# Performance work log

Hardware: AMD Instinct MI355X
Metric: run time of the kernel (lower is better)

Reference implementation:

```python
import jax, jax.numpy as jnp
import numpy as np

PRE_NMS_TOPK = 6000
POST_NMS_TOPK = 1000
NMS_THRESH = 0.7
MIN_SIZE = 16.0
NEG = -1e9  # stand-in for -inf that is safe under autodiff


def setup_inputs() -> dict:
    key = jax.random.key(0)
    k1, k2, k3, k4, k5, k6, k7, k8 = jax.random.split(key, 8)
    B, A = 8, 200000
    N = B * A
    # realistic anchors: centers within a ~1333x800 canvas, sizes 16..256
    cx = jax.random.uniform(k1, (N,), minval=0.0, maxval=1200.0)
    cy = jax.random.uniform(k2, (N,), minval=0.0, maxval=800.0)
    w = jax.random.uniform(k3, (N,), minval=16.0, maxval=256.0)
    h = jax.random.uniform(k4, (N,), minval=16.0, maxval=256.0)
    anchors = jnp.stack([cx - 0.5 * w, cy - 0.5 * h, cx + 0.5 * w, cy + 0.5 * h], axis=1)
    batch_indices = jnp.sort(jax.random.randint(k5, (N,), 0, B)).astype(jnp.int32)
    image_sizes = jax.random.randint(k6, (B, 2), 600, 1334).astype(jnp.int32)  # (H, W)
    objectness_logits = jax.random.normal(k7, (N, 1), dtype=jnp.float32)
    bbox_deltas = jax.random.normal(k8, (N, 4), dtype=jnp.float32) * 0.2
    return {
        'anchors': anchors,
        'batch_indices': batch_indices,
        'image_sizes': image_sizes,
        'objectness_logits': objectness_logits,
        'bbox_deltas': bbox_deltas,
    }


def _nms_one(bx, sc):
    """Greedy NMS on [K,4] boxes / [K] scores; returns POST_NMS_TOPK (idx, ok)."""
    K = bx.shape[0]
    areas = (bx[:, 2] - bx[:, 0]) * (bx[:, 3] - bx[:, 1])
    ar = jnp.arange(K)

    def step(sup, _):
        s = jnp.where(sup, NEG, sc)
        j = jnp.argmax(s)
        ok = s[j] > 0.5 * NEG
        b = bx[j]
        ix1 = jnp.maximum(b[0], bx[:, 0])
        iy1 = jnp.maximum(b[1], bx[:, 1])
        ix2 = jnp.minimum(b[2], bx[:, 2])
        iy2 = jnp.minimum(b[3], bx[:, 3])
        inter = jnp.maximum(ix2 - ix1, 0.0) * jnp.maximum(iy2 - iy1, 0.0)
        iou = inter / (areas + areas[j] - inter + 1e-9)
        sup = sup | (iou > NMS_THRESH) | (ar == j)
        return sup, (j, ok)

    sup0 = sc <= 0.5 * NEG  # padded / invalid entries start suppressed
    _, (idx, ok) = jax.lax.scan(step, sup0, None, length=POST_NMS_TOPK)
    return idx, ok


def reference(anchors, batch_indices, image_sizes, objectness_logits, bbox_deltas):
    B = image_sizes.shape[0]
    N = anchors.shape[0]
    sizes = image_sizes[batch_indices].astype(jnp.float32)  # [N,2] (H,W) per anchor

    # --- box decode ---
    a_w = anchors[:, 2] - anchors[:, 0]
    a_h = anchors[:, 3] - anchors[:, 1]
    a_x = anchors[:, 0] + 0.5 * a_w
    a_y = anchors[:, 1] + 0.5 * a_h
    t_x, t_y = bbox_deltas[:, 0], bbox_deltas[:, 1]
    t_w, t_h = bbox_deltas[:, 2], bbox_deltas[:, 3]
    p_x = a_x + t_x * a_w
    p_y = a_y + t_y * a_h
    p_w = a_w * jnp.exp(jnp.clip(t_w, -10.0, 10.0))
    p_h = a_h * jnp.exp(jnp.clip(t_h, -10.0, 10.0))
    x1 = p_x - 0.5 * p_w
    y1 = p_y - 0.5 * p_h
    x2 = p_x + 0.5 * p_w
    y2 = p_y + 0.5 * p_h

    # --- clip to image ---
    H, W = sizes[:, 0], sizes[:, 1]
    x1 = jnp.clip(x1, 0.0, W - 1.0)
    y1 = jnp.clip(y1, 0.0, H - 1.0)
    x2 = jnp.clip(x2, 0.0, W - 1.0)
    y2 = jnp.clip(y2, 0.0, H - 1.0)
    boxes = jnp.stack([x1, y1, x2, y2], axis=1)  # [N,4]

    # --- min-size filter (as score masking) ---
    valid = ((x2 - x1) >= MIN_SIZE) & ((y2 - y1) >= MIN_SIZE)
    fg = jax.nn.sigmoid(objectness_logits[:, 0])

    # --- per-image top-k over masked scores ---
    img_mask = batch_indices[None, :] == jnp.arange(B, dtype=batch_indices.dtype)[:, None]  # [B,N]
    scores = jnp.where(img_mask & valid[None, :], fg[None, :], NEG)  # [B,N]
    top_scores, top_idx = jax.lax.top_k(scores, PRE_NMS_TOPK)  # [B,PRE]
    top_boxes = boxes[top_idx]  # [B,PRE,4]

    # --- NMS per image ---
    keep_idx, keep_ok = jax.vmap(_nms_one)(top_boxes, top_scores)  # [B,POST]

    sel = jnp.take_along_axis(top_idx, keep_idx, axis=1)  # global anchor indices [B,POST]
    okf = keep_ok[..., None].astype(boxes.dtype)
    props = jnp.take_along_axis(top_boxes, keep_idx[..., None], axis=1) * okf  # [B,POST,4]
    obj = objectness_logits[sel] * okf  # [B,POST,1]
    deltas_out = bbox_deltas[sel] * okf  # [B,POST,4]
    bidx = jnp.where(keep_ok, jnp.arange(B, dtype=jnp.int32)[:, None], -1)  # [B,POST]

    return (props.reshape(-1, 4), bidx.reshape(-1), obj.reshape(-1, 1),
            deltas_out.reshape(-1, 4), keep_ok.reshape(-1))
```

## Files before the change

### kernel.cpp

```cpp
#include <hip/hip_runtime.h>
#include <stdint.h>

#define PRE_K   6000
#define POST_K  1000
#define CAP     8192
#define BINS    1024
#define ROWS    6016
#define CH      94
#define RC_CH   32
#define JSPLIT  4
#define NEGF    -1000000000.0f
#define IOU_EPS 16.0f


__device__ __forceinline__ uint32_t orderf(float f) {
  uint32_t u = __float_as_uint(f);
  return (u & 0x80000000u) ? ~u : (u | 0x80000000u);
}

__device__ __forceinline__ int score_bin(float sc) {
  int bin = (int)floorf((sc + 12.0f) * ((float)BINS / 24.0f));
  return bin < 0 ? 0 : (bin > BINS - 1 ? BINS - 1 : bin);
}

__device__ __forceinline__ int bin_slot(int bin) {
  return ((bin & 15) << 6) | (bin >> 4);
}

__device__ __forceinline__ void decode_box(
    const float* __restrict__ anchors, const float* __restrict__ deltas,
    const int* __restrict__ isz, int n, int b,
    double& x1, double& y1, double& x2, double& y2, bool& valid) {
  double ax1 = (double)anchors[4 * n + 0], ay1 = (double)anchors[4 * n + 1];
  double ax2 = (double)anchors[4 * n + 2], ay2 = (double)anchors[4 * n + 3];
  double aw = ax2 - ax1, ah = ay2 - ay1;
  double acx = ax1 + 0.5 * aw, acy = ay1 + 0.5 * ah;
  double tx = (double)deltas[4 * n + 0], ty = (double)deltas[4 * n + 1];
  double tw = (double)deltas[4 * n + 2], th = (double)deltas[4 * n + 3];
  tw = tw < -10.0 ? -10.0 : (tw > 10.0 ? 10.0 : tw);
  th = th < -10.0 ? -10.0 : (th > 10.0 ? 10.0 : th);
  double px = acx + tx * aw, py = acy + ty * ah;
  double pw = aw * exp(tw), ph = ah * exp(th);
  double H = (double)isz[2 * b + 0], W = (double)isz[2 * b + 1];
  double wm = W - 1.0, hm = H - 1.0;
  x1 = px - 0.5 * pw; y1 = py - 0.5 * ph;
  x2 = px + 0.5 * pw; y2 = py + 0.5 * ph;
  x1 = fmin(fmax(x1, 0.0), wm); x2 = fmin(fmax(x2, 0.0), wm);
  y1 = fmin(fmax(y1, 0.0), hm); y2 = fmin(fmax(y2, 0.0), hm);
  valid = (x2 - x1 >= 16.0) && (y2 - y1 >= 16.0);
}

__device__ __forceinline__ bool iou_exact(const double* __restrict__ tbox,
                                          const double* __restrict__ tarea,
                                          size_t ri, size_t ci) {
  const double* pr = &tbox[ri * 4];
  const double* pc = &tbox[ci * 4];
  double w = fmin(pr[2], pc[2]) - fmax(pr[0], pc[0]); w = w > 0.0 ? w : 0.0;
  double h = fmin(pr[3], pc[3]) - fmax(pr[1], pc[1]); h = h > 0.0 ? h : 0.0;
  double it = w * h;
  return it > 0.7 * (tarea[ri] + tarea[ci] - it + 1e-9);
}


__global__ void k_init(uint32_t* hist, uint32_t* cnt, uint32_t* prank, int B) {
  int i = blockIdx.x * blockDim.x + threadIdx.x;
  if (i < B * BINS) hist[i] = 0u;
  if (i < B) cnt[i] = 0u;
  if (i < B * CAP) prank[i] = 0u;
}

__global__ void __launch_bounds__(256) k_score(const float* __restrict__ anchors,
                                               const int* __restrict__ bix,
                                               const int* __restrict__ isz,
                                               const float* __restrict__ logits,
                                               const float* __restrict__ deltas,
                                               float* __restrict__ scores,
                                               uint32_t* __restrict__ hist, int N) {
  const int SPAN = 4096;
  int start = blockIdx.x * SPAN;
  int end = start + SPAN < N ? start + SPAN : N;
  __shared__ uint32_t lh[2][BINS];
  for (int i = threadIdx.x; i < 2 * BINS; i += 256) ((uint32_t*)lh)[i] = 0u;
  __shared__ int s_b0, s_b1;
  if (threadIdx.x == 0) { s_b0 = bix[start]; s_b1 = bix[end - 1]; }
  __syncthreads();
  int b0 = s_b0, b1 = s_b1;

  for (int n = start + (int)threadIdx.x; n < end; n += 256) {
    int b = bix[n];
    double x1, y1, x2, y2; bool valid;
    decode_box(anchors, deltas, isz, n, b, x1, y1, x2, y2, valid);
    float sc = valid ? logits[n] : NEGF;
    scores[n] = sc;
    if (valid) {
      int bin = score_bin(sc);
      if (b == b0)      atomicAdd(&lh[0][bin], 1u);
      else if (b == b1) atomicAdd(&lh[1][bin], 1u);
      else              atomicAdd(&hist[b * BINS + bin_slot(bin)], 1u);
    }
  }
  __syncthreads();
  for (int bin = threadIdx.x; bin < BINS; bin += 256) {
    uint32_t c0 = lh[0][bin];
    if (c0) atomicAdd(&hist[b0 * BINS + bin_slot(bin)], c0);
    if (b1 != b0) {
      uint32_t c1 = lh[1][bin];
      if (c1) atomicAdd(&hist[b1 * BINS + bin_slot(bin)], c1);
    }
  }
}

__global__ void k_scan(const uint32_t* __restrict__ hist, uint32_t* __restrict__ bstar) {
  __shared__ uint32_t s[BINS];
  __shared__ int bs;
  int b = blockIdx.x, t = threadIdx.x;
  s[t] = hist[b * BINS + bin_slot(t)];
  if (t == 0) bs = 0;
  __syncthreads();
  for (int off = 1; off < BINS; off <<= 1) {
    uint32_t v = (t + off < BINS) ? s[t + off] : 0u;
    __syncthreads();
    s[t] += v;
    __syncthreads();
  }
  if (s[t] >= PRE_K) atomicMax(&bs, t);
  __syncthreads();
  if (t == 0) bstar[b] = (uint32_t)bs;
}

__global__ void __launch_bounds__(1024) k_compact(const float* __restrict__ scores,
                                                  const int* __restrict__ bix,
                                                  const uint32_t* __restrict__ bstar,
                                                  uint32_t* __restrict__ cnt,
                                                  uint64_t* __restrict__ cand, int N) {
  const int SPAN = 8192;
  int start = blockIdx.x * SPAN;
  int end = start + SPAN < N ? start + SPAN : N;
  __shared__ uint32_t lcnt[8], lbase[8];
  if (threadIdx.x < 8) lcnt[threadIdx.x] = 0u;
  __syncthreads();

  bool     predv[8];
  uint64_t keyv[8];
  uint32_t lposv[8];
  int      bv[8];
  int nt = 0;
  for (int base = start; base < end; base += 1024, nt++) {
    int n = base + (int)threadIdx.x;
    bool pred = false; int b = 0; uint64_t key = 0ull; uint32_t lp = 0u;
    if (n < end) {
      float sc = scores[n];
      if (sc > 0.5f * NEGF) {
        b = bix[n];
        if ((uint32_t)score_bin(sc) >= bstar[b]) {
          pred = true;
          key = ((uint64_t)orderf(sc) << 32) | (uint64_t)(uint32_t)(~(uint32_t)n);
          lp = atomicAdd(&lcnt[b], 1u);
        }
      }
    }
    predv[nt] = pred; keyv[nt] = key; lposv[nt] = lp; bv[nt] = b;
  }
  __syncthreads();
  if (threadIdx.x < 8) {
    uint32_t c = lcnt[threadIdx.x];
    lbase[threadIdx.x] = c ? atomicAdd(&cnt[threadIdx.x], c) : 0u;
  }
  __syncthreads();
  for (int k = 0; k < nt; k++) {
    if (predv[k]) {
      uint32_t pos = lbase[bv[k]] + lposv[k];
      if (pos < CAP) cand[(size_t)bv[k] * CAP + pos] = keyv[k];
    }
  }
}

__global__ void __launch_bounds__(256) k_rank(const uint64_t* __restrict__ cand,
                                              const uint32_t* __restrict__ cnt,
                                              uint32_t* __restrict__ prank) {
  int blk = blockIdx.x;
  int js = blk % JSPLIT;
  int ic = (blk / JSPLIT) % 32;
  int b  = blk / (JSPLIT * 32);
  int t = threadIdx.x;
  int C = (int)min(cnt[b], (uint32_t)CAP);
  if (ic * 256 >= C) return;
  const uint64_t* g = cand + (size_t)b * CAP;
  int i = ic * 256 + t;
  uint64_t ki = (i < C) ? g[i] : 0ull;

  int q = (C + JSPLIT - 1) / JSPLIT;
  int j0 = js * q;
  int j1 = j0 + q < C ? j0 + q : C;
  if (j0 >= j1) return;

  __shared__ uint64_t tile[1024];
  int rank = 0;
  for (int base = j0; base < j1; base += 1024) {
#pragma unroll
    for (int u = 0; u < 4; u++) {
      int j = base + u * 256 + t;
      tile[u * 256 + t] = (j < j1) ? g[j] : 0ull;
    }
    __syncthreads();
    int lim = j1 - base < 1024 ? j1 - base : 1024;
    const ulonglong2* t2 = (const ulonglong2*)tile;
    int pairs = lim >> 1;
    int jj = 0;
    for (; jj + 4 <= pairs; jj += 4) {
      ulonglong2 v0 = t2[jj + 0], v1 = t2[jj + 1];
      ulonglong2 v2 = t2[jj + 2], v3 = t2[jj + 3];
      rank += (v0.x > ki) ? 1 : 0; rank += (v0.y > ki) ? 1 : 0;
      rank += (v1.x > ki) ? 1 : 0; rank += (v1.y > ki) ? 1 : 0;
      rank += (v2.x > ki) ? 1 : 0; rank += (v2.y > ki) ? 1 : 0;
      rank += (v3.x > ki) ? 1 : 0; rank += (v3.y > ki) ? 1 : 0;
    }
    for (; jj < pairs; jj++) {
      ulonglong2 v = t2[jj];
      rank += (v.x > ki) ? 1 : 0; rank += (v.y > ki) ? 1 : 0;
    }
    if (lim & 1) rank += (tile[lim - 1] > ki) ? 1 : 0;
    __syncthreads();
  }
  if (i < C && rank) atomicAdd(&prank[b * CAP + i], (uint32_t)rank);
}

__global__ void __launch_bounds__(256) k_place(const uint64_t* __restrict__ cand,
                                               const uint32_t* __restrict__ cnt,
                                               const uint32_t* __restrict__ prank,
                                               int* __restrict__ sorted_n,
                                               int* __restrict__ Cnum, int B) {
  int idx = blockIdx.x * blockDim.x + threadIdx.x;
  if (idx >= B * CAP) return;
  int b = idx / CAP, i = idx % CAP;
  int C = (int)min(cnt[b], (uint32_t)CAP);
  if (i == 0) Cnum[b] = C < PRE_K ? C : PRE_K;
  if (i >= C) return;
  uint32_t rank = prank[idx];
  if (rank < PRE_K)
    sorted_n[b * PRE_K + rank] =
        (int)(~(uint32_t)(cand[(size_t)b * CAP + i] & 0xFFFFFFFFull));
}

__global__ void k_gather(const float* __restrict__ anchors,
                         const float* __restrict__ deltas,
                         const int* __restrict__ isz,
                         const int* __restrict__ sorted_n,
                         const int* __restrict__ Cnum,
                         double* __restrict__ tbox, double* __restrict__ tarea,
                         float4* __restrict__ tboxf, float* __restrict__ tareaf,
                         int* __restrict__ top_n, int B) {
  int idx = blockIdx.x * blockDim.x + threadIdx.x;
  if (idx >= B * PRE_K) return;
  int b = idx / PRE_K, r = idx % PRE_K;
  if (r >= Cnum[b]) return;
  int n = sorted_n[idx];
  double x1, y1, x2, y2; bool valid;
  decode_box(anchors, deltas, isz, n, b, x1, y1, x2, y2, valid);
  size_t row = (size_t)b * ROWS + r;
  tbox[row * 4 + 0] = x1;
  tbox[row * 4 + 1] = y1;
  tbox[row * 4 + 2] = x2;
  tbox[row * 4 + 3] = y2;
  double ar = (x2 - x1) * (y2 - y1);
  tarea[row] = ar;
  tboxf[row] = make_float4((float)x1, (float)y1, (float)x2, (float)y2);
  tareaf[row] = (float)ar;
  top_n[idx] = n;
}

__global__ void __launch_bounds__(64) k_iou_mat(const float4* __restrict__ tboxf,
                                                const float* __restrict__ tareaf,
                                                const double* __restrict__ tbox,
                                                const double* __restrict__ tarea,
                                                const int* __restrict__ Cnum,
                                                uint32_t* __restrict__ maskT) {
  int blk = blockIdx.x;
  int k  = blk % (RC_CH + 1);
  int cc = (blk / (RC_CH + 1)) % CH;
  int b  = blk / ((RC_CH + 1) * CH);
  int rc = (k == RC_CH) ? cc : k;
  if (k < RC_CH && cc <= rc) return;
  int C = Cnum[b];
  if (rc * 64 >= C || cc * 64 >= C) return;
  int lane = threadIdx.x;
  size_t bb = (size_t)b * ROWS;

  float4 cb4 = tboxf[bb + (size_t)cc * 64 + lane];
  float  cba = tareaf[bb + (size_t)cc * 64 + lane];
  __shared__ float4 rbx[64];
  __shared__ float  rba[64];
  rbx[lane] = tboxf[bb + (size_t)rc * 64 + lane];
  rba[lane] = tareaf[bb + (size_t)rc * 64 + lane];
  __syncthreads();

  uint32_t* seg = maskT + (((size_t)b * CH + cc) * ROWS + (size_t)rc * 64) * 2;
  bool isdiag = (rc == cc);

  for (int i = 0; i < 64; i++) {
    float4 r4 = rbx[i];
    float ra = rba[i];
    float iw = fminf(r4.z, cb4.z) - fmaxf(r4.x, cb4.x);
    float ih = fminf(r4.w, cb4.w) - fmaxf(r4.y, cb4.y);
    iw = fmaxf(iw, 0.0f); ih = fmaxf(ih, 0.0f);
    float inter = iw * ih;
    float diff = inter - 0.7f * (ra + cba - inter);
    bool gt = isdiag ? (lane > i) : true;
    unsigned long long sup   = __ballot(gt && (diff >  IOU_EPS));
    unsigned long long loose = __ballot(gt && (diff > -IOU_EPS));
    unsigned long long border = loose & ~sup;
    if (border) {
      bool mine = (border >> lane) & 1ull;
      bool ex = false;
      if (mine)
        ex = iou_exact(tbox, tarea, bb + (size_t)rc * 64 + i,
                       bb + (size_t)cc * 64 + lane);
      sup |= __ballot(ex);
    }
    if (lane == 0) {
      seg[i * 2 + 0] = (uint32_t)sup;
      seg[i * 2 + 1] = (uint32_t)(sup >> 32);
    }
  }
}

__global__ void __launch_bounds__(256) k_nms_reduce(const uint32_t* __restrict__ maskT,
                                                    const float4* __restrict__ tboxf,
                                                    const float* __restrict__ tareaf,
                                                    const double* __restrict__ tbox,
                                                    const double* __restrict__ tarea,
                                                    const int* __restrict__ Cnum,
                                                    int* __restrict__ keep,
                                                    int* __restrict__ kept_count) {
  int b = blockIdx.x, t = threadIdx.x;
  int wave = t >> 6, lane = t & 63;
  int C = Cnum[b];
  const uint32_t* M = maskT + (size_t)b * CH * ROWS * 2;
  size_t bb = (size_t)b * ROWS;

  __shared__ uint32_t s_f[2][2];
  __shared__ uint32_t kept_lo[POST_K];
  __shared__ uint32_t kept_hi[POST_K];
  __shared__ uint64_t s_kept;
  if (t < 4) ((uint32_t*)s_f)[t] = 0u;

  uint32_t d0 = 0u, d1 = 0u;
  if (wave == 0) {
    const uint32_t* rp = M + (size_t)lane * 2;
    d0 = rp[0]; d1 = rp[1];
  }
  __syncthreads();

  int nkept = 0, nlo = 0, nhi = 0;
  for (int c = 0; c < CH; c++) {
    int base = c * 64;
    if (base >= C) break;
    int cbuf = c & 1;
    if (t == 0) { s_f[cbuf ^ 1][0] = 0u; s_f[cbuf ^ 1][1] = 0u; }

    uint32_t f0 = 0u, f1 = 0u;
    for (int k2 = t; k2 < nlo; k2 += 256) {
      const uint32_t* rp = M + ((size_t)c * ROWS + kept_lo[k2]) * 2;
      f0 |= rp[0]; f1 |= rp[1];
    }
    if (wave == 1 && nhi > 0) {
      float4 cb4 = tboxf[bb + base + lane];
      float  cba = tareaf[bb + base + lane];
      for (int k2 = 0; k2 < nhi; k2++) {
        int r = (int)kept_hi[k2];
        float4 r4 = tboxf[bb + r];
        float ra = tareaf[bb + r];
        float iw = fminf(r4.z, cb4.z) - fmaxf(r4.x, cb4.x);
        float ih = fminf(r4.w, cb4.w) - fmaxf(r4.y, cb4.y);
        iw = fmaxf(iw, 0.0f); ih = fmaxf(ih, 0.0f);
        float inter = iw * ih;
        float diff = inter - 0.7f * (ra + cba - inter);
        unsigned long long sup   = __ballot(diff >  IOU_EPS);
        unsigned long long loose = __ballot(diff > -IOU_EPS);
        unsigned long long border = loose & ~sup;
        if (border) {
          bool mine = (border >> lane) & 1ull;
          bool ex = false;
          if (mine) ex = iou_exact(tbox, tarea, bb + r, bb + base + lane);
          sup |= __ballot(ex);
        }
        f0 |= (uint32_t)sup; f1 |= (uint32_t)(sup >> 32);
      }
    }
#pragma unroll
    for (int off = 32; off > 0; off >>= 1) {
      f0 |= (uint32_t)__shfl_xor((int)f0, off, 64);
      f1 |= (uint32_t)__shfl_xor((int)f1, off, 64);
    }
    if (lane == 0 && (f0 | f1)) {
      atomicOr(&s_f[cbuf][0], f0);
      atomicOr(&s_f[cbuf][1], f1);
    }
    __syncthreads();

    if (wave == 0) {
      uint64_t sup = (uint64_t)s_f[cbuf][0] | ((uint64_t)s_f[cbuf][1] << 32);
      int rem = C - base;
      if (rem < 64) sup |= ~((1ull << rem) - 1ull);
      uint64_t diag = (uint64_t)d0 | ((uint64_t)d1 << 32);
      int cn = (c + 1 < CH) ? c + 1 : c;
      const uint32_t* rpn = M + ((size_t)cn * ROWS + (size_t)cn * 64 + lane) * 2;
      uint32_t pn0 = rpn[0], pn1 = rpn[1];

      uint64_t keptMask = 0ull;
      uint64_t alive = ~sup;
      uint64_t m = alive;
      while (m) {
        int i = __builtin_ctzll(m);
        keptMask |= 1ull << i;
        uint64_t d = (uint64_t)__shfl((long long)diag, i, 64);
        sup |= d | (1ull << i);
        m = alive & ~sup;
      }
      int allowed = POST_K - nkept;
      int pc = __popcll(keptMask);
      while (pc > allowed) {
        keptMask &= ~(1ull << (63 - __builtin_clzll(keptMask)));
        pc--;
      }
      if (lane == 0) s_kept = keptMask;
      if ((keptMask >> lane) & 1ull) {
        int pfx = __popcll(keptMask & ((1ull << lane) - 1ull));
        keep[b * POST_K + nkept + pfx] = base + lane;
        if (c < RC_CH) kept_lo[nlo + pfx] = (uint32_t)(base + lane);
        else           kept_hi[nhi + pfx] = (uint32_t)(base + lane);
      }
      d0 = pn0; d1 = pn1;
    }
    __syncthreads();

    int pc = __popcll(s_kept);
    nkept += pc;
    if (c < RC_CH) nlo += pc; else nhi += pc;
    if (nkept >= POST_K) break;
  }
  if (t == 0) kept_count[b] = nkept;
}

__global__ void k_output(const int* __restrict__ keep,
                         const int* __restrict__ kept_count,
                         const int* __restrict__ top_n,
                         const double* __restrict__ tbox,
                         const float* __restrict__ logits,
                         const float* __restrict__ deltas,
                         float* __restrict__ out, int B) {
  int idx = blockIdx.x * blockDim.x + threadIdx.x;
  int M = B * POST_K;
  if (idx >= M) return;
  int b = idx / POST_K, s = idx % POST_K;
  float p0 = 0.f, p1 = 0.f, p2 = 0.f, p3 = 0.f;
  float ob = 0.f, d0 = 0.f, d1 = 0.f, d2 = 0.f, d3 = 0.f;
  float bi = -1.0f, okv = 0.0f;
  if (s < kept_count[b]) {
    int j = keep[b * POST_K + s];
    int n = top_n[b * PRE_K + j];
    const double* p = &tbox[((size_t)b * ROWS + j) * 4];
    p0 = (float)p[0]; p1 = (float)p[1]; p2 = (float)p[2]; p3 = (float)p[3];
    ob = logits[n];
    d0 = deltas[4 * n + 0]; d1 = deltas[4 * n + 1];
    d2 = deltas[4 * n + 2]; d3 = deltas[4 * n + 3];
    bi = (float)b; okv = 1.0f;
  }
  out[idx * 4 + 0] = p0;
  out[idx * 4 + 1] = p1;
  out[idx * 4 + 2] = p2;
  out[idx * 4 + 3] = p3;
  out[4 * M + idx] = bi;
  out[5 * M + idx] = ob;
  out[6 * M + idx * 4 + 0] = d0;
  out[6 * M + idx * 4 + 1] = d1;
  out[6 * M + idx * 4 + 2] = d2;
  out[6 * M + idx * 4 + 3] = d3;
  out[10 * M + idx] = okv;
}


extern "C" void kernel_launch(void* const* d_in, const int* in_sizes, int n_in,
                              void* d_out, int out_size, void* d_ws, size_t ws_size,
                              hipStream_t stream) {
  const float* anchors = (const float*)d_in[0];
  const int*   bix     = (const int*)d_in[1];
  const int*   isz     = (const int*)d_in[2];
  const float* logits  = (const float*)d_in[3];
  const float* deltas  = (const float*)d_in[4];
  float* out = (float*)d_out;

  int N = in_sizes[1];
  int B = in_sizes[2] / 2;

  uintptr_t p = (uintptr_t)d_ws;
  double*   tbox   = (double*)p;    p += (size_t)B * ROWS * 4 * sizeof(double);
  double*   tarea  = (double*)p;    p += (size_t)B * ROWS * sizeof(double);
  uint64_t* cand   = (uint64_t*)p;  p += (size_t)B * CAP * sizeof(uint64_t);
  float*    scores = (float*)p;     p += (size_t)N * sizeof(float);
  uint32_t* hist   = (uint32_t*)p;  p += (size_t)B * BINS * sizeof(uint32_t);
  uint32_t* prank  = (uint32_t*)p;  p += (size_t)B * CAP * sizeof(uint32_t);
  int*      sorted_n = (int*)p;     p += (size_t)B * PRE_K * sizeof(int);
  int*      top_n    = (int*)p;     p += (size_t)B * PRE_K * sizeof(int);
  int*      keep     = (int*)p;     p += (size_t)B * POST_K * sizeof(int);
  uint32_t* cnt      = (uint32_t*)p; p += (size_t)B * sizeof(uint32_t);
  uint32_t* bstar    = (uint32_t*)p; p += (size_t)B * sizeof(uint32_t);
  int*      Cnum     = (int*)p;      p += (size_t)B * sizeof(int);
  int*      kept_cnt = (int*)p;      p += (size_t)B * sizeof(int);
  p = (p + 255) & ~(uintptr_t)255;
  uint32_t* maskT    = (uint32_t*)p; p += (size_t)B * CH * ROWS * 2 * sizeof(uint32_t);
  float4*   tboxf  = (float4*)scores;
  float*    tareaf = (float*)(scores + (size_t)B * ROWS * 4);
  (void)ws_size; (void)n_in; (void)out_size;

  int initN = B * CAP;
  k_init<<<(initN + 255) / 256, 256, 0, stream>>>(hist, cnt, prank, B);
  k_score<<<(N + 4095) / 4096, 256, 0, stream>>>(anchors, bix, isz, logits, deltas,
                                                 scores, hist, N);
  k_scan<<<B, BINS, 0, stream>>>(hist, bstar);
  k_compact<<<(N + 8191) / 8192, 1024, 0, stream>>>(scores, bix, bstar, cnt, cand, N);
  k_rank<<<B * 32 * JSPLIT, 256, 0, stream>>>(cand, cnt, prank);
  k_place<<<(B * CAP + 255) / 256, 256, 0, stream>>>(cand, cnt, prank,
                                                     sorted_n, Cnum, B);
  k_gather<<<(B * PRE_K + 255) / 256, 256, 0, stream>>>(anchors, deltas, isz,
                                                        sorted_n, Cnum, tbox,
                                                        tarea, tboxf, tareaf,
                                                        top_n, B);
  k_iou_mat<<<B * CH * (RC_CH + 1), 64, 0, stream>>>(tboxf, tareaf, tbox, tarea,
                                                     Cnum, maskT);
  k_nms_reduce<<<B, 256, 0, stream>>>(maskT, tboxf, tareaf, tbox, tarea, Cnum,
                                      keep, kept_cnt);
  k_output<<<(B * POST_K + 255) / 256, 256, 0, stream>>>(keep, kept_cnt, top_n,
                                                         tbox, logits, deltas,
                                                         out, B);
}
```

Measured before the change: 358.9 us.

## Fuse place and gather kernels; compute full upper-triangle IoU mask, drop on-the-fly IoU

Merges the rank-placement and box-gather kernels into one, so each candidate decodes its box and writes it straight to its ranked row, with no sorted_n intermediate and one fewer launch. The IoU mask kernel now covers the full upper triangle of chunk pairs instead of only the first 32 row chunks. The serial NMS reduce therefore only ORs precomputed mask rows and no longer recomputes IoU against late kept boxes inside the sequential loop. The cost is a much larger IoU grid, many of whose blocks exit early, plus extra mask memory traffic for chunks the reduce may never reach once 1000 boxes are kept.

```diff
diff --git a/kernel.cpp b/kernel.cpp
--- a/kernel.cpp
+++ b/kernel.cpp
@@ -7,7 +7,6 @@
 #define BINS    1024
 #define ROWS    6016
 #define CH      94
-#define RC_CH   32
 #define JSPLIT  4
 #define NEGF    -1000000000.0f
 #define IOU_EPS 16.0f
@@ -225,11 +224,14 @@
   if (i < C && rank) atomicAdd(&prank[b * CAP + i], (uint32_t)rank);
 }
 
-__global__ void __launch_bounds__(256) k_place(const uint64_t* __restrict__ cand,
-                                               const uint32_t* __restrict__ cnt,
-                                               const uint32_t* __restrict__ prank,
-                                               int* __restrict__ sorted_n,
-                                               int* __restrict__ Cnum, int B) {
+__global__ void __launch_bounds__(256) k_place_gather(
+    const uint64_t* __restrict__ cand, const uint32_t* __restrict__ cnt,
+    const uint32_t* __restrict__ prank,
+    const float* __restrict__ anchors, const float* __restrict__ deltas,
+    const int* __restrict__ isz,
+    double* __restrict__ tbox, double* __restrict__ tarea,
+    float4* __restrict__ tboxf, float* __restrict__ tareaf,
+    int* __restrict__ top_n, int* __restrict__ Cnum, int B) {
   int idx = blockIdx.x * blockDim.x + threadIdx.x;
   if (idx >= B * CAP) return;
   int b = idx / CAP, i = idx % CAP;
@@ -237,27 +239,11 @@
   if (i == 0) Cnum[b] = C < PRE_K ? C : PRE_K;
   if (i >= C) return;
   uint32_t rank = prank[idx];
-  if (rank < PRE_K)
-    sorted_n[b * PRE_K + rank] =
-        (int)(~(uint32_t)(cand[(size_t)b * CAP + i] & 0xFFFFFFFFull));
-}
-
-__global__ void k_gather(const float* __restrict__ anchors,
-                         const float* __restrict__ deltas,
-                         const int* __restrict__ isz,
-                         const int* __restrict__ sorted_n,
-                         const int* __restrict__ Cnum,
-                         double* __restrict__ tbox, double* __restrict__ tarea,
-                         float4* __restrict__ tboxf, float* __restrict__ tareaf,
-                         int* __restrict__ top_n, int B) {
-  int idx = blockIdx.x * blockDim.x + threadIdx.x;
-  if (idx >= B * PRE_K) return;
-  int b = idx / PRE_K, r = idx % PRE_K;
-  if (r >= Cnum[b]) return;
-  int n = sorted_n[idx];
+  if (rank >= PRE_K) return;
+  int n = (int)(~(uint32_t)(cand[idx] & 0xFFFFFFFFull));
   double x1, y1, x2, y2; bool valid;
   decode_box(anchors, deltas, isz, n, b, x1, y1, x2, y2, valid);
-  size_t row = (size_t)b * ROWS + r;
+  size_t row = (size_t)b * ROWS + rank;
   tbox[row * 4 + 0] = x1;
   tbox[row * 4 + 1] = y1;
   tbox[row * 4 + 2] = x2;
@@ -266,7 +252,7 @@
   tarea[row] = ar;
   tboxf[row] = make_float4((float)x1, (float)y1, (float)x2, (float)y2);
   tareaf[row] = (float)ar;
-  top_n[idx] = n;
+  top_n[b * PRE_K + rank] = n;
 }
 
 __global__ void __launch_bounds__(64) k_iou_mat(const float4* __restrict__ tboxf,
@@ -276,11 +262,10 @@
                                                 const int* __restrict__ Cnum,
                                                 uint32_t* __restrict__ maskT) {
   int blk = blockIdx.x;
-  int k  = blk % (RC_CH + 1);
-  int cc = (blk / (RC_CH + 1)) % CH;
-  int b  = blk / ((RC_CH + 1) * CH);
-  int rc = (k == RC_CH) ? cc : k;
-  if (k < RC_CH && cc <= rc) return;
+  int cc = blk % CH;
+  int rc = (blk / CH) % CH;
+  int b  = blk / (CH * CH);
+  if (cc < rc) return;
   int C = Cnum[b];
   if (rc * 64 >= C || cc * 64 >= C) return;
   int lane = threadIdx.x;
@@ -325,10 +310,6 @@
 }
 
 __global__ void __launch_bounds__(256) k_nms_reduce(const uint32_t* __restrict__ maskT,
-                                                    const float4* __restrict__ tboxf,
-                                                    const float* __restrict__ tareaf,
-                                                    const double* __restrict__ tbox,
-                                                    const double* __restrict__ tarea,
                                                     const int* __restrict__ Cnum,
                                                     int* __restrict__ keep,
                                                     int* __restrict__ kept_count) {
@@ -336,11 +317,9 @@
   int wave = t >> 6, lane = t & 63;
   int C = Cnum[b];
   const uint32_t* M = maskT + (size_t)b * CH * ROWS * 2;
-  size_t bb = (size_t)b * ROWS;
 
   __shared__ uint32_t s_f[2][2];
-  __shared__ uint32_t kept_lo[POST_K];
-  __shared__ uint32_t kept_hi[POST_K];
+  __shared__ uint32_t kept_s[POST_K];
   __shared__ uint64_t s_kept;
   if (t < 4) ((uint32_t*)s_f)[t] = 0u;
 
@@ -351,7 +330,7 @@
   }
   __syncthreads();
 
-  int nkept = 0, nlo = 0, nhi = 0;
+  int nkept = 0;
   for (int c = 0; c < CH; c++) {
     int base = c * 64;
     if (base >= C) break;
@@ -359,33 +338,9 @@
     if (t == 0) { s_f[cbuf ^ 1][0] = 0u; s_f[cbuf ^ 1][1] = 0u; }
 
     uint32_t f0 = 0u, f1 = 0u;
-    for (int k2 = t; k2 < nlo; k2 += 256) {
-      const uint32_t* rp = M + ((size_t)c * ROWS + kept_lo[k2]) * 2;
+    for (int k2 = t; k2 < nkept; k2 += 256) {
+      const uint32_t* rp = M + ((size_t)c * ROWS + kept_s[k2]) * 2;
       f0 |= rp[0]; f1 |= rp[1];
-    }
-    if (wave == 1 && nhi > 0) {
-      float4 cb4 = tboxf[bb + base + lane];
-      float  cba = tareaf[bb + base + lane];
-      for (int k2 = 0; k2 < nhi; k2++) {
-        int r = (int)kept_hi[k2];
-        float4 r4 = tboxf[bb + r];
-        float ra = tareaf[bb + r];
-        float iw = fminf(r4.z, cb4.z) - fmaxf(r4.x, cb4.x);
-        float ih = fminf(r4.w, cb4.w) - fmaxf(r4.y, cb4.y);
-        iw = fmaxf(iw, 0.0f); ih = fmaxf(ih, 0.0f);
-        float inter = iw * ih;
-        float diff = inter - 0.7f * (ra + cba - inter);
-        unsigned long long sup   = __ballot(diff >  IOU_EPS);
-        unsigned long long loose = __ballot(diff > -IOU_EPS);
-        unsigned long long border = loose & ~sup;
-        if (border) {
-          bool mine = (border >> lane) & 1ull;
-          bool ex = false;
-          if (mine) ex = iou_exact(tbox, tarea, bb + r, bb + base + lane);
-          sup |= __ballot(ex);
-        }
-        f0 |= (uint32_t)sup; f1 |= (uint32_t)(sup >> 32);
-      }
     }
 #pragma unroll
     for (int off = 32; off > 0; off >>= 1) {
@@ -427,16 +382,13 @@
       if ((keptMask >> lane) & 1ull) {
         int pfx = __popcll(keptMask & ((1ull << lane) - 1ull));
         keep[b * POST_K + nkept + pfx] = base + lane;
-        if (c < RC_CH) kept_lo[nlo + pfx] = (uint32_t)(base + lane);
-        else           kept_hi[nhi + pfx] = (uint32_t)(base + lane);
+        kept_s[nkept + pfx] = (uint32_t)(base + lane);
       }
       d0 = pn0; d1 = pn1;
     }
     __syncthreads();
 
-    int pc = __popcll(s_kept);
-    nkept += pc;
-    if (c < RC_CH) nlo += pc; else nhi += pc;
+    nkept += __popcll(s_kept);
     if (nkept >= POST_K) break;
   }
   if (t == 0) kept_count[b] = nkept;
@@ -500,7 +452,6 @@
   float*    scores = (float*)p;     p += (size_t)N * sizeof(float);
   uint32_t* hist   = (uint32_t*)p;  p += (size_t)B * BINS * sizeof(uint32_t);
   uint32_t* prank  = (uint32_t*)p;  p += (size_t)B * CAP * sizeof(uint32_t);
-  int*      sorted_n = (int*)p;     p += (size_t)B * PRE_K * sizeof(int);
   int*      top_n    = (int*)p;     p += (size_t)B * PRE_K * sizeof(int);
   int*      keep     = (int*)p;     p += (size_t)B * POST_K * sizeof(int);
   uint32_t* cnt      = (uint32_t*)p; p += (size_t)B * sizeof(uint32_t);
@@ -520,16 +471,12 @@
   k_scan<<<B, BINS, 0, stream>>>(hist, bstar);
   k_compact<<<(N + 8191) / 8192, 1024, 0, stream>>>(scores, bix, bstar, cnt, cand, N);
   k_rank<<<B * 32 * JSPLIT, 256, 0, stream>>>(cand, cnt, prank);
-  k_place<<<(B * CAP + 255) / 256, 256, 0, stream>>>(cand, cnt, prank,
-                                                     sorted_n, Cnum, B);
-  k_gather<<<(B * PRE_K + 255) / 256, 256, 0, stream>>>(anchors, deltas, isz,
-                                                        sorted_n, Cnum, tbox,
-                                                        tarea, tboxf, tareaf,
-                                                        top_n, B);
-  k_iou_mat<<<B * CH * (RC_CH + 1), 64, 0, stream>>>(tboxf, tareaf, tbox, tarea,
-                                                     Cnum, maskT);
-  k_nms_reduce<<<B, 256, 0, stream>>>(maskT, tboxf, tareaf, tbox, tarea, Cnum,
-                                      keep, kept_cnt);
+  k_place_gather<<<(B * CAP + 255) / 256, 256, 0, stream>>>(cand, cnt, prank,
+                                                            anchors, deltas, isz,
+                                                            tbox, tarea, tboxf,
+                                                            tareaf, top_n, Cnum, B);
+  k_iou_mat<<<B * CH * CH, 64, 0, stream>>>(tboxf, tareaf, tbox, tarea, Cnum, maskT);
+  k_nms_reduce<<<B, 256, 0, stream>>>(maskT, Cnum, keep, kept_cnt);
   k_output<<<(B * POST_K + 255) / 256, 256, 0, stream>>>(keep, kept_cnt, top_n,
                                                          tbox, logits, deltas,
                                                          out, B);
```

After: 398.8 us. 1.11x slower.

## Fuse place and gather kernels, coalesce mask writes, spread NMS tail across waves

Applied to the files above, without the earlier changes.

Merges k_place and k_gather into one kernel that decodes each box straight into its rank slot, which removes the sorted_n round trip and one launch. In k_iou_mat, each lane now keeps its own row's suppression mask and writes it once as a coalesced uint2 store, replacing 64 serial single-lane stores. The IoU test is rewritten as one FMA with pre-scaled areas. In k_nms_reduce, the per-chunk loop over high kept boxes is split across all four waves instead of running on one. The rewritten threshold can round slightly differently near the boundary, but the exact double-precision fallback band is still there.

```diff
diff --git a/kernel.cpp b/kernel.cpp
--- a/kernel.cpp
+++ b/kernel.cpp
@@ -225,11 +225,14 @@
   if (i < C && rank) atomicAdd(&prank[b * CAP + i], (uint32_t)rank);
 }
 
-__global__ void __launch_bounds__(256) k_place(const uint64_t* __restrict__ cand,
-                                               const uint32_t* __restrict__ cnt,
-                                               const uint32_t* __restrict__ prank,
-                                               int* __restrict__ sorted_n,
-                                               int* __restrict__ Cnum, int B) {
+__global__ void __launch_bounds__(256) k_place_gather(
+    const uint64_t* __restrict__ cand, const uint32_t* __restrict__ cnt,
+    const uint32_t* __restrict__ prank,
+    const float* __restrict__ anchors, const float* __restrict__ deltas,
+    const int* __restrict__ isz,
+    double* __restrict__ tbox, double* __restrict__ tarea,
+    float4* __restrict__ tboxf, float* __restrict__ tareaf,
+    int* __restrict__ top_n, int* __restrict__ Cnum, int B) {
   int idx = blockIdx.x * blockDim.x + threadIdx.x;
   if (idx >= B * CAP) return;
   int b = idx / CAP, i = idx % CAP;
@@ -237,27 +240,11 @@
   if (i == 0) Cnum[b] = C < PRE_K ? C : PRE_K;
   if (i >= C) return;
   uint32_t rank = prank[idx];
-  if (rank < PRE_K)
-    sorted_n[b * PRE_K + rank] =
-        (int)(~(uint32_t)(cand[(size_t)b * CAP + i] & 0xFFFFFFFFull));
-}
-
-__global__ void k_gather(const float* __restrict__ anchors,
-                         const float* __restrict__ deltas,
-                         const int* __restrict__ isz,
-                         const int* __restrict__ sorted_n,
-                         const int* __restrict__ Cnum,
-                         double* __restrict__ tbox, double* __restrict__ tarea,
-                         float4* __restrict__ tboxf, float* __restrict__ tareaf,
-                         int* __restrict__ top_n, int B) {
-  int idx = blockIdx.x * blockDim.x + threadIdx.x;
-  if (idx >= B * PRE_K) return;
-  int b = idx / PRE_K, r = idx % PRE_K;
-  if (r >= Cnum[b]) return;
-  int n = sorted_n[idx];
+  if (rank >= PRE_K) return;
+  int n = (int)(~(uint32_t)(cand[idx] & 0xFFFFFFFFull));
   double x1, y1, x2, y2; bool valid;
   decode_box(anchors, deltas, isz, n, b, x1, y1, x2, y2, valid);
-  size_t row = (size_t)b * ROWS + r;
+  size_t row = (size_t)b * ROWS + rank;
   tbox[row * 4 + 0] = x1;
   tbox[row * 4 + 1] = y1;
   tbox[row * 4 + 2] = x2;
@@ -266,7 +253,7 @@
   tarea[row] = ar;
   tboxf[row] = make_float4((float)x1, (float)y1, (float)x2, (float)y2);
   tareaf[row] = (float)ar;
-  top_n[idx] = n;
+  top_n[b * PRE_K + rank] = n;
 }
 
 __global__ void __launch_bounds__(64) k_iou_mat(const float4* __restrict__ tboxf,
@@ -287,24 +274,24 @@
   size_t bb = (size_t)b * ROWS;
 
   float4 cb4 = tboxf[bb + (size_t)cc * 64 + lane];
-  float  cba = tareaf[bb + (size_t)cc * 64 + lane];
+  float  sca = 0.7f * tareaf[bb + (size_t)cc * 64 + lane];
   __shared__ float4 rbx[64];
-  __shared__ float  rba[64];
+  __shared__ float  rsa[64];
   rbx[lane] = tboxf[bb + (size_t)rc * 64 + lane];
-  rba[lane] = tareaf[bb + (size_t)rc * 64 + lane];
-  __syncthreads();
-
-  uint32_t* seg = maskT + (((size_t)b * CH + cc) * ROWS + (size_t)rc * 64) * 2;
+  rsa[lane] = 0.7f * tareaf[bb + (size_t)rc * 64 + lane];
+  __syncthreads();
+
   bool isdiag = (rc == cc);
+  uint32_t res0 = 0u, res1 = 0u;
 
   for (int i = 0; i < 64; i++) {
     float4 r4 = rbx[i];
-    float ra = rba[i];
+    float sra = rsa[i];
     float iw = fminf(r4.z, cb4.z) - fmaxf(r4.x, cb4.x);
     float ih = fminf(r4.w, cb4.w) - fmaxf(r4.y, cb4.y);
     iw = fmaxf(iw, 0.0f); ih = fmaxf(ih, 0.0f);
     float inter = iw * ih;
-    float diff = inter - 0.7f * (ra + cba - inter);
+    float diff = fmaf(1.7f, inter, -(sra + sca));
     bool gt = isdiag ? (lane > i) : true;
     unsigned long long sup   = __ballot(gt && (diff >  IOU_EPS));
     unsigned long long loose = __ballot(gt && (diff > -IOU_EPS));
@@ -317,11 +304,10 @@
                        bb + (size_t)cc * 64 + lane);
       sup |= __ballot(ex);
     }
-    if (lane == 0) {
-      seg[i * 2 + 0] = (uint32_t)sup;
-      seg[i * 2 + 1] = (uint32_t)(sup >> 32);
-    }
-  }
+    if (lane == i) { res0 = (uint32_t)sup; res1 = (uint32_t)(sup >> 32); }
+  }
+  uint2* seg = (uint2*)(maskT + (((size_t)b * CH + cc) * ROWS + (size_t)rc * 64) * 2);
+  seg[lane] = make_uint2(res0, res1);
 }
 
 __global__ void __launch_bounds__(256) k_nms_reduce(const uint32_t* __restrict__ maskT,
@@ -363,18 +349,18 @@
       const uint32_t* rp = M + ((size_t)c * ROWS + kept_lo[k2]) * 2;
       f0 |= rp[0]; f1 |= rp[1];
     }
-    if (wave == 1 && nhi > 0) {
+    if (nhi > 0) {
       float4 cb4 = tboxf[bb + base + lane];
-      float  cba = tareaf[bb + base + lane];
-      for (int k2 = 0; k2 < nhi; k2++) {
+      float  sca = 0.7f * tareaf[bb + base + lane];
+      for (int k2 = wave; k2 < nhi; k2 += 4) {
         int r = (int)kept_hi[k2];
         float4 r4 = tboxf[bb + r];
-        float ra = tareaf[bb + r];
+        float sra = 0.7f * tareaf[bb + r];
         float iw = fminf(r4.z, cb4.z) - fmaxf(r4.x, cb4.x);
         float ih = fminf(r4.w, cb4.w) - fmaxf(r4.y, cb4.y);
         iw = fmaxf(iw, 0.0f); ih = fmaxf(ih, 0.0f);
         float inter = iw * ih;
-        float diff = inter - 0.7f * (ra + cba - inter);
+        float diff = fmaf(1.7f, inter, -(sra + sca));
         unsigned long long sup   = __ballot(diff >  IOU_EPS);
         unsigned long long loose = __ballot(diff > -IOU_EPS);
         unsigned long long border = loose & ~sup;
@@ -500,7 +486,6 @@
   float*    scores = (float*)p;     p += (size_t)N * sizeof(float);
   uint32_t* hist   = (uint32_t*)p;  p += (size_t)B * BINS * sizeof(uint32_t);
   uint32_t* prank  = (uint32_t*)p;  p += (size_t)B * CAP * sizeof(uint32_t);
-  int*      sorted_n = (int*)p;     p += (size_t)B * PRE_K * sizeof(int);
   int*      top_n    = (int*)p;     p += (size_t)B * PRE_K * sizeof(int);
   int*      keep     = (int*)p;     p += (size_t)B * POST_K * sizeof(int);
   uint32_t* cnt      = (uint32_t*)p; p += (size_t)B * sizeof(uint32_t);
@@ -520,12 +505,10 @@
   k_scan<<<B, BINS, 0, stream>>>(hist, bstar);
   k_compact<<<(N + 8191) / 8192, 1024, 0, stream>>>(scores, bix, bstar, cnt, cand, N);
   k_rank<<<B * 32 * JSPLIT, 256, 0, stream>>>(cand, cnt, prank);
-  k_place<<<(B * CAP + 255) / 256, 256, 0, stream>>>(cand, cnt, prank,
-                                                     sorted_n, Cnum, B);
-  k_gather<<<(B * PRE_K + 255) / 256, 256, 0, stream>>>(anchors, deltas, isz,
-                                                        sorted_n, Cnum, tbox,
-                                                        tarea, tboxf, tareaf,
-                                                        top_n, B);
+  k_place_gather<<<(B * CAP + 255) / 256, 256, 0, stream>>>(cand, cnt, prank,
+                                                            anchors, deltas, isz,
+                                                            tbox, tarea, tboxf,
+                                                            tareaf, top_n, Cnum, B);
   k_iou_mat<<<B * CH * (RC_CH + 1), 64, 0, stream>>>(tboxf, tareaf, tbox, tarea,
                                                      Cnum, maskT);
   k_nms_reduce<<<B, 256, 0, stream>>>(maskT, tboxf, tareaf, tbox, tarea, Cnum,
```

Result: no change. 354.9 us (-1.1%).
